# Optimization experiments

Hardware: AMD Instinct MI355X
Metric: run time of the kernel (lower is better)

Reference implementation:

```python
import jax, jax.numpy as jnp
import numpy as np

N, E, F_IN, EDGE_DIM = 50000, 800000, 128, 64
H, C = 4, 64  # heads, per-head out channels
NEG_SLOPE = 0.2  # PyG GATConv default


def setup_inputs() -> dict:
    key = jax.random.key(0)
    ks = jax.random.split(key, 16)
    p = lambda i, shape: jax.random.normal(ks[i], shape, jnp.float32) * 0.05
    return {
        "node_features": jax.random.normal(ks[0], (N, F_IN), jnp.float32),
        "edge_features": jax.random.normal(ks[1], (E, EDGE_DIM), jnp.float32),
        "edge_index": jax.random.randint(ks[2], (2, E), 0, N),
        # layer 1 (concat=True, ELU)
        "W1": p(3, (F_IN, H * C)),
        "att_src1": p(4, (H, C)), "att_dst1": p(5, (H, C)), "att_edge1": p(6, (H, C)),
        "bias1": jnp.zeros((H * C,), jnp.float32),
        "edgeW1": p(7, (EDGE_DIM, H * C)),
        # layer 2 (concat=False -> mean over heads, no activation)
        "W2": p(8, (H * C, H * C)),
        "att_src2": p(9, (H, C)), "att_dst2": p(10, (H, C)), "att_edge2": p(11, (H, C)),
        "bias2": jnp.zeros((C,), jnp.float32),
        "edgeW2": p(12, (EDGE_DIM, H * C)),
    }


def _gat_layer(x, edge_feat, src, dst, W, a_s, a_d, a_e, bias, edgeW, concat):
    n = x.shape[0]
    h = (x @ W).reshape(n, H, C)                      # [N,H,C]
    ef = (edge_feat @ edgeW).reshape(-1, H, C)        # [E,H,C] edge_linear projection
    # GATConv add_self_loops=True, fill_value='mean': self-loop attr = mean of incoming edge attrs
    ones = jnp.ones((src.shape[0],), x.dtype)
    cnt = jnp.maximum(jax.ops.segment_sum(ones, dst, num_segments=n), 1.0)
    loop_attr = jax.ops.segment_sum(ef, dst, num_segments=n) / cnt[:, None, None]
    ef_f = jnp.concatenate([ef, loop_attr], axis=0)   # [E+N,H,C]
    loops = jnp.arange(n)
    src_f = jnp.concatenate([src, loops], axis=0)
    dst_f = jnp.concatenate([dst, loops], axis=0)
    # per-edge attention logits: alpha_j + alpha_i + alpha_edge
    a_src = jnp.einsum('nhc,hc->nh', h, a_s)
    a_dst = jnp.einsum('nhc,hc->nh', h, a_d)
    logits = a_src[src_f] + a_dst[dst_f] + jnp.einsum('ehc,hc->eh', ef_f, a_e)
    logits = jax.nn.leaky_relu(logits, NEG_SLOPE)     # [E+N,H]
    # segment softmax over incoming edges of each dst node (every node has a self-loop)
    m = jax.ops.segment_max(logits, dst_f, num_segments=n)
    pexp = jnp.exp(logits - m[dst_f])
    denom = jax.ops.segment_sum(pexp, dst_f, num_segments=n)
    alpha = pexp / (denom[dst_f] + 1e-16)
    # message = x_j * alpha, scatter-add to dst
    out = jax.ops.segment_sum(h[src_f] * alpha[..., None], dst_f, num_segments=n)  # [N,H,C]
    if concat:
        return out.reshape(n, H * C) + bias
    return out.mean(axis=1) + bias


def reference(node_features, edge_features, edge_index,
              W1, att_src1, att_dst1, att_edge1, bias1, edgeW1,
              W2, att_src2, att_dst2, att_edge2, bias2, edgeW2):
    src, dst = edge_index[0], edge_index[1]
    x = _gat_layer(node_features, edge_features, src, dst,
                   W1, att_src1, att_dst1, att_edge1, bias1, edgeW1, concat=True)
    x = jax.nn.elu(x)
    return _gat_layer(x, edge_features, src, dst,
                      W2, att_src2, att_dst2, att_edge2, bias2, edgeW2, concat=False)
```

## Files before the change

kernel.cpp:

```cpp
#include <hip/hip_runtime.h>
#include <hip/hip_fp16.h>
#include <math.h>

#define NNODE 50000
#define NEDGE 800000
#define FIN 128
#define EDIM 64
#define HC 256
#define NH 4
#define CC 64
#define SCAN_TILE 512

typedef _Float16 half8v __attribute__((ext_vector_type(8)));
typedef _Float16 half4v __attribute__((ext_vector_type(4)));
typedef float floatx4 __attribute__((ext_vector_type(4)));

__global__ __launch_bounds__(256) void k_prep(int* counts, int* cursor,
                                              const float* __restrict__ W1, _Float16* wt1,
                                              const float* __restrict__ W2, _Float16* wt2,
                                              const float* __restrict__ eW1, const float* __restrict__ ae1, float* we1,
                                              const float* __restrict__ eW2, const float* __restrict__ ae2, float* we2) {
    int b = blockIdx.x, t = threadIdx.x;
    if (b < 391) {
        int i = b * 256 + t;
        if (i < NNODE) counts[i] = 0;
        else if (i < 2 * NNODE) cursor[i - NNODE] = 0;
    } else if (b < 519) {
        int idx = (b - 391) * 256 + t;
        int n = idx >> 7, k = idx & 127;
        wt1[n * FIN + k] = (_Float16)W1[(size_t)k * HC + n];
    } else if (b < 775) {
        int idx = (b - 519) * 256 + t;
        int n = idx >> 8, k = idx & 255;
        wt2[n * HC + k] = (_Float16)W2[(size_t)k * HC + n];
    } else {
        int idx = (b - 775) * 256 + t;
        const float* eW = idx < 256 ? eW1 : eW2;
        const float* ae = idx < 256 ? ae1 : ae2;
        float* we = idx < 256 ? we1 : we2;
        int q = idx & 255;
        int d = q >> 2, hh = q & 3;
        float s = 0.f;
        for (int c = 0; c < 64; c++) s += eW[d * HC + hh * 64 + c] * ae[hh * 64 + c];
        we[d * 4 + hh] = s;
    }
}

__global__ void k_count(const int* __restrict__ dst, int* counts, int E) {
    int e = blockIdx.x * 256 + threadIdx.x;
    if (e < E) atomicAdd(&counts[dst[e]], 1);
}

__global__ void k_scan1(const int* __restrict__ counts, int* offs, int* tilesums, int N) {
    __shared__ int s[SCAN_TILE];
    int t = threadIdx.x;
    int i = blockIdx.x * SCAN_TILE + t;
    int v = (i < N) ? counts[i] : 0;
    s[t] = v;
    for (int off = 1; off < SCAN_TILE; off <<= 1) {
        __syncthreads();
        int x = (t >= off) ? s[t - off] : 0;
        __syncthreads();
        s[t] += x;
    }
    __syncthreads();
    if (i < N) offs[i] = s[t] - v;
    if (t == SCAN_TILE - 1) tilesums[blockIdx.x] = s[t];
}

__global__ void k_scan2(int* tilesums, int nt) {
    __shared__ int s[128];
    int t = threadIdx.x;
    int v = (t < nt) ? tilesums[t] : 0;
    s[t] = v;
    for (int off = 1; off < 128; off <<= 1) {
        __syncthreads();
        int x = (t >= off) ? s[t - off] : 0;
        __syncthreads();
        s[t] += x;
    }
    __syncthreads();
    if (t < nt) tilesums[t] = s[t] - v;
}

__global__ void k_scan3(int* offs, const int* __restrict__ tilesums, int N, int E) {
    int t = threadIdx.x;
    int i = blockIdx.x * SCAN_TILE + t;
    if (i < N) offs[i] += tilesums[blockIdx.x];
    if (i == 0) offs[N] = E;
}

__global__ void k_fill(const int* __restrict__ src, const int* __restrict__ dst,
                       const int* __restrict__ offs, int* cursor,
                       int2* __restrict__ es, int E) {
    int e = blockIdx.x * 256 + threadIdx.x;
    if (e < E) {
        int d = dst[e];
        int pos = offs[d] + atomicAdd(&cursor[d], 1);
        es[pos] = make_int2(e, src[e]);
    }
}

__device__ inline float4 h4_to_f4(uint2 r) {
    float2 fa = __half22float2(*(__half2*)&r.x);
    float2 fb = __half22float2(*(__half2*)&r.y);
    return make_float4(fa.x, fa.y, fb.x, fb.y);
}

__device__ inline float sel_h(float4 v, int head) {
    return head == 0 ? v.x : head == 1 ? v.y : head == 2 ? v.z : v.w;
}

template <typename AT>
__global__ __launch_bounds__(256) void k_gemm_mfma(const AT* __restrict__ A,
                                                   const _Float16* __restrict__ Wt16,
                                                   _Float16* __restrict__ H16,
                                                   const float* __restrict__ att_s,
                                                   const float* __restrict__ att_d,
                                                   float* __restrict__ asrc,
                                                   float* __restrict__ adst,
                                                   int M, int K) {
    int wave = threadIdx.x >> 6, lane = threadIdx.x & 63;
    int quad = lane >> 4, l16 = lane & 15;
    int row = blockIdx.x * 64 + wave * 16 + l16;
    bool rok = row < M;
    floatx4 acc[16];
#pragma unroll
    for (int i = 0; i < 16; i++) acc[i] = (floatx4)(0.0f);
    int nk = K >> 5;
    for (int kk = 0; kk < nk; kk++) {
        half8v a = {};
        if (rok) {
            if constexpr (sizeof(AT) == 2) {
                a = *(const half8v*)(A + (size_t)row * K + kk * 32 + quad * 8);
            } else {
                const float* ap = (const float*)A + (size_t)row * K + kk * 32 + quad * 8;
                float4 v0 = *(const float4*)ap;
                float4 v1 = *(const float4*)(ap + 4);
                a[0] = (_Float16)v0.x; a[1] = (_Float16)v0.y;
                a[2] = (_Float16)v0.z; a[3] = (_Float16)v0.w;
                a[4] = (_Float16)v1.x; a[5] = (_Float16)v1.y;
                a[6] = (_Float16)v1.z; a[7] = (_Float16)v1.w;
            }
        }
#pragma unroll
        for (int nt = 0; nt < 16; nt++) {
            half8v b = *(const half8v*)(Wt16 + (size_t)(nt * 16 + l16) * K + kk * 32 + quad * 8);
            acc[nt] = __builtin_amdgcn_mfma_f32_16x16x32_f16(a, b, acc[nt], 0, 0, 0);
        }
    }
    float asl[16], adl[16];
#pragma unroll
    for (int nt = 0; nt < 16; nt++) {
        asl[nt] = att_s[nt * 16 + l16];
        adl[nt] = att_d[nt * 16 + l16];
    }
    int orow0 = blockIdx.x * 64 + wave * 16 + quad * 4;
#pragma unroll
    for (int r = 0; r < 4; r++) {
        int orow = orow0 + r;
        float4 vs4, vd4;
        float* vsp = (float*)&vs4;
        float* vdp = (float*)&vd4;
#pragma unroll
        for (int hh = 0; hh < 4; hh++) {
            float vs = 0.f, vd = 0.f;
#pragma unroll
            for (int q = 0; q < 4; q++) {
                int nt = hh * 4 + q;
                float hv = acc[nt][r];
                vs += hv * asl[nt];
                vd += hv * adl[nt];
            }
            vs += __shfl_xor(vs, 1, 64); vd += __shfl_xor(vd, 1, 64);
            vs += __shfl_xor(vs, 2, 64); vd += __shfl_xor(vd, 2, 64);
            vs += __shfl_xor(vs, 4, 64); vd += __shfl_xor(vd, 4, 64);
            vs += __shfl_xor(vs, 8, 64); vd += __shfl_xor(vd, 8, 64);
            vsp[hh] = vs; vdp[hh] = vd;
        }
        if (l16 == 0 && orow < M) {
            ((float4*)asrc)[orow] = vs4;
            ((float4*)adst)[orow] = vd4;
        }
    }
#pragma unroll
    for (int r = 0; r < 4; r++) {
        int orow = orow0 + r;
        if (orow < M) {
#pragma unroll
            for (int nt = 0; nt < 16; nt++)
                H16[(size_t)orow * HC + nt * 16 + l16] = (_Float16)acc[nt][r];
        }
    }
}

__global__ __launch_bounds__(256) void k_elog_both(const float* __restrict__ ef,
                                                   const float* __restrict__ we1,
                                                   const float* __restrict__ we2,
                                                   const int2* __restrict__ es,
                                                   float* __restrict__ elogc1,
                                                   float* __restrict__ elogc2, int E) {
    __shared__ float sw1[256], sw2[256];
    int t = threadIdx.x;
    sw1[t] = we1[t];
    sw2[t] = we2[t];
    __syncthreads();
    int p = blockIdx.x * 256 + t;
    if (p >= E) return;
    int e = es[p].x;
    const float4* row = (const float4*)(ef + (size_t)(uint)e * EDIM);
    float a10 = 0.f, a11 = 0.f, a12 = 0.f, a13 = 0.f;
    float a20 = 0.f, a21 = 0.f, a22 = 0.f, a23 = 0.f;
#pragma unroll
    for (int c4 = 0; c4 < 16; c4++) {
        float4 v = row[c4];
        const float* vp = (const float*)&v;
#pragma unroll
        for (int k = 0; k < 4; k++) {
            float vv = vp[k];
            int c = c4 * 4 + k;
            float4 w1 = *(const float4*)&sw1[c << 2];
            float4 w2 = *(const float4*)&sw2[c << 2];
            a10 += vv * w1.x; a11 += vv * w1.y; a12 += vv * w1.z; a13 += vv * w1.w;
            a20 += vv * w2.x; a21 += vv * w2.y; a22 += vv * w2.z; a23 += vv * w2.w;
        }
    }
    ((float4*)elogc1)[p] = make_float4(a10, a11, a12, a13);
    ((float4*)elogc2)[p] = make_float4(a20, a21, a22, a23);
}

template <int LAYER>
__global__ __launch_bounds__(256) void k_aggr_fused(const _Float16* __restrict__ hb,
                                                    const float* __restrict__ elogc,
                                                    const float* __restrict__ asrc,
                                                    const float* __restrict__ adst,
                                                    const int* __restrict__ offs,
                                                    const int2* __restrict__ es,
                                                    const float* __restrict__ bias,
                                                    _Float16* __restrict__ out16,
                                                    float* __restrict__ out32, int N) {
    __shared__ float sW[4][256];
    int wave = threadIdx.x >> 6, lane = threadIdx.x & 63;
    int n = blockIdx.x * 4 + wave;
    if (n >= N) return;
    int head = lane >> 4;
    const uint2* hf = (const uint2*)hb;
    const float4* elc = (const float4*)elogc;
    const float4* asp = (const float4*)asrc;
    float* sWp = sW[wave];
    int beg = offs[n], end = offs[n + 1];

    float4 adn = ((const float4*)adst)[n];
    float adnh = sel_h(adn, head);

    float denom = 0.f;
    float sx = 0.f, sy = 0.f, sz = 0.f, sw = 0.f;
    float ax = 0.f, ay = 0.f, az = 0.f, aw = 0.f;

    for (int i0 = beg; i0 < end; i0 += 64) {
        int m = end - i0; if (m > 64) m = 64;
        bool act = lane < m;
        int sj = 0;
        float4 el = make_float4(0.f, 0.f, 0.f, 0.f);
        float4 a4 = make_float4(0.f, 0.f, 0.f, 0.f);
        if (act) {
            uint idx = (uint)(i0 + lane);
            sj = es[idx].y;
            el = elc[idx];
            a4 = asp[(uint)sj];
        }
        sx += el.x; sy += el.y; sz += el.z; sw += el.w;
        float4 w4;
        float l;
        l = a4.x + adn.x + el.x; l = l > 0.f ? l : 0.2f * l; w4.x = act ? __expf(l) : 0.f;
        l = a4.y + adn.y + el.y; l = l > 0.f ? l : 0.2f * l; w4.y = act ? __expf(l) : 0.f;
        l = a4.z + adn.z + el.z; l = l > 0.f ? l : 0.2f * l; w4.z = act ? __expf(l) : 0.f;
        l = a4.w + adn.w + el.w; l = l > 0.f ? l : 0.2f * l; w4.w = act ? __expf(l) : 0.f;
        *(float4*)&sWp[lane << 2] = w4;
        __builtin_amdgcn_wave_barrier();

        int j = 0;
        for (; j + 16 <= m; j += 16) {
            uint2 r[16];
            float w[16];
#pragma unroll
            for (int k = 0; k < 16; k++) {
                int sk = __builtin_amdgcn_readlane(sj, j + k);
                w[k] = sWp[((j + k) << 2) + head];
                r[k] = hf[(size_t)((uint)sk * 64u) + lane];
            }
#pragma unroll
            for (int k = 0; k < 16; k++) {
                float4 h4 = h4_to_f4(r[k]);
                denom += w[k];
                ax += w[k] * h4.x; ay += w[k] * h4.y;
                az += w[k] * h4.z; aw += w[k] * h4.w;
            }
        }
        for (; j + 8 <= m; j += 8) {
            uint2 r[8];
            float w[8];
#pragma unroll
            for (int k = 0; k < 8; k++) {
                int sk = __builtin_amdgcn_readlane(sj, j + k);
                w[k] = sWp[((j + k) << 2) + head];
                r[k] = hf[(size_t)((uint)sk * 64u) + lane];
            }
#pragma unroll
            for (int k = 0; k < 8; k++) {
                float4 h4 = h4_to_f4(r[k]);
                denom += w[k];
                ax += w[k] * h4.x; ay += w[k] * h4.y;
                az += w[k] * h4.z; aw += w[k] * h4.w;
            }
        }
        for (; j < m; j++) {
            int sk = __builtin_amdgcn_readlane(sj, j);
            float wk = sWp[(j << 2) + head];
            uint2 rk = hf[(size_t)((uint)sk * 64u) + lane];
            float4 h4 = h4_to_f4(rk);
            denom += wk;
            ax += wk * h4.x; ay += wk * h4.y;
            az += wk * h4.z; aw += wk * h4.w;
        }
        __builtin_amdgcn_wave_barrier();
    }

#pragma unroll
    for (int msk = 32; msk >= 1; msk >>= 1) {
        sx += __shfl_xor(sx, msk, 64);
        sy += __shfl_xor(sy, msk, 64);
        sz += __shfl_xor(sz, msk, 64);
        sw += __shfl_xor(sw, msk, 64);
    }
    float selh = sel_h(make_float4(sx, sy, sz, sw), head);

    float cnt = (float)(end - beg);
    if (cnt < 1.f) cnt = 1.f;
    float asnh = sel_h(asp[(uint)n], head);
    float ls = asnh + adnh + selh / cnt;
    ls = ls > 0.f ? ls : 0.2f * ls;
    float ws = __expf(ls);
    denom += ws;
    float4 hn = h4_to_f4(hf[(size_t)n * 64 + lane]);
    ax += ws * hn.x; ay += ws * hn.y; az += ws * hn.z; aw += ws * hn.w;

    float inv = 1.0f / (denom + 1e-16f);
    ax *= inv; ay *= inv; az *= inv; aw *= inv;

    if (LAYER == 1) {
        float4 bv = ((const float4*)bias)[lane];
        half4v o;
        float v;
        v = ax + bv.x; o[0] = (_Float16)(v > 0.f ? v : __expf(v) - 1.0f);
        v = ay + bv.y; o[1] = (_Float16)(v > 0.f ? v : __expf(v) - 1.0f);
        v = az + bv.z; o[2] = (_Float16)(v > 0.f ? v : __expf(v) - 1.0f);
        v = aw + bv.w; o[3] = (_Float16)(v > 0.f ? v : __expf(v) - 1.0f);
        ((half4v*)(out16 + (size_t)n * HC))[lane] = o;
    } else {
        ax += __shfl_xor(ax, 16, 64); ax += __shfl_xor(ax, 32, 64);
        ay += __shfl_xor(ay, 16, 64); ay += __shfl_xor(ay, 32, 64);
        az += __shfl_xor(az, 16, 64); az += __shfl_xor(az, 32, 64);
        aw += __shfl_xor(aw, 16, 64); aw += __shfl_xor(aw, 32, 64);
        if (lane < 16) {
            float4 bv = ((const float4*)bias)[lane];
            float4 o;
            o.x = 0.25f * ax + bv.x;
            o.y = 0.25f * ay + bv.y;
            o.z = 0.25f * az + bv.z;
            o.w = 0.25f * aw + bv.w;
            ((float4*)(out32 + (size_t)n * CC))[lane] = o;
        }
    }
}

extern "C" void kernel_launch(void* const* d_in, const int* in_sizes, int n_in,
                              void* d_out, int out_size, void* d_ws, size_t ws_size,
                              hipStream_t stream) {
    const float* x   = (const float*)d_in[0];
    const float* ef  = (const float*)d_in[1];
    const int*   ei  = (const int*)d_in[2];
    const float* W1  = (const float*)d_in[3];
    const float* as1 = (const float*)d_in[4];
    const float* ad1 = (const float*)d_in[5];
    const float* ae1 = (const float*)d_in[6];
    const float* b1  = (const float*)d_in[7];
    const float* eW1 = (const float*)d_in[8];
    const float* W2  = (const float*)d_in[9];
    const float* as2 = (const float*)d_in[10];
    const float* ad2 = (const float*)d_in[11];
    const float* ae2 = (const float*)d_in[12];
    const float* b2  = (const float*)d_in[13];
    const float* eW2 = (const float*)d_in[14];
    float* out = (float*)d_out;
    const int* srcp = ei;
    const int* dstp = ei + NEDGE;

    char* w = (char*)d_ws;
    auto alloc = [&](size_t bytes) -> char* {
        char* r = w;
        w += (bytes + 255) / 256 * 256;
        return r;
    };
    _Float16* hb16  = (_Float16*)alloc((size_t)NNODE * HC * 2);
    _Float16* x216  = (_Float16*)alloc((size_t)NNODE * HC * 2);
    _Float16* wt1   = (_Float16*)alloc((size_t)HC * FIN * 2);
    _Float16* wt2   = (_Float16*)alloc((size_t)HC * HC * 2);
    float* elogc1 = (float*)alloc((size_t)NEDGE * 4 * 4);
    float* elogc2 = (float*)alloc((size_t)NEDGE * 4 * 4);
    float* asrc   = (float*)alloc((size_t)NNODE * 4 * 4);
    float* adst   = (float*)alloc((size_t)NNODE * 4 * 4);
    float* webuf1 = (float*)alloc(64 * 4 * 4);
    float* webuf2 = (float*)alloc(64 * 4 * 4);
    int* counts  = (int*)alloc((size_t)NNODE * 4);
    int* offs    = (int*)alloc((size_t)(NNODE + 1) * 4);
    int* tiles   = (int*)alloc(1024 * 4);
    int* cursor  = (int*)alloc((size_t)NNODE * 4);
    int2* es     = (int2*)alloc((size_t)NEDGE * 8);

    k_prep<<<777, 256, 0, stream>>>(counts, cursor, W1, wt1, W2, wt2,
                                    eW1, ae1, webuf1, eW2, ae2, webuf2);

    k_count<<<(NEDGE + 255) / 256, 256, 0, stream>>>(dstp, counts, NEDGE);
    int nt = (NNODE + SCAN_TILE - 1) / SCAN_TILE;
    k_scan1<<<nt, SCAN_TILE, 0, stream>>>(counts, offs, tiles, NNODE);
    k_scan2<<<1, 128, 0, stream>>>(tiles, nt);
    k_scan3<<<nt, SCAN_TILE, 0, stream>>>(offs, tiles, NNODE, NEDGE);
    k_fill<<<(NEDGE + 255) / 256, 256, 0, stream>>>(srcp, dstp, offs, cursor, es, NEDGE);

    k_elog_both<<<(NEDGE + 255) / 256, 256, 0, stream>>>(ef, webuf1, webuf2, es, elogc1, elogc2, NEDGE);

    k_gemm_mfma<float><<<(NNODE + 63) / 64, 256, 0, stream>>>(x, wt1, hb16, as1, ad1, asrc, adst, NNODE, FIN);
    k_aggr_fused<1><<<(NNODE + 3) / 4, 256, 0, stream>>>(hb16, elogc1, asrc, adst, offs, es, b1, x216, nullptr, NNODE);

    k_gemm_mfma<_Float16><<<(NNODE + 63) / 64, 256, 0, stream>>>(x216, wt2, hb16, as2, ad2, asrc, adst, NNODE, HC);
    k_aggr_fused<2><<<(NNODE + 3) / 4, 256, 0, stream>>>(hb16, elogc2, asrc, adst, offs, es, b2, nullptr, out, NNODE);
}
```

Baseline: 702.9 us.

## Record atomic rank in count pass and fuse CSR fill with edge-logit computation

```diff
diff --git a/kernel.cpp b/kernel.cpp
--- a/kernel.cpp
+++ b/kernel.cpp
@@ -15,26 +15,25 @@
 typedef _Float16 half4v __attribute__((ext_vector_type(4)));
 typedef float floatx4 __attribute__((ext_vector_type(4)));
 
-__global__ __launch_bounds__(256) void k_prep(int* counts, int* cursor,
+__global__ __launch_bounds__(256) void k_prep(int* counts,
                                               const float* __restrict__ W1, _Float16* wt1,
                                               const float* __restrict__ W2, _Float16* wt2,
                                               const float* __restrict__ eW1, const float* __restrict__ ae1, float* we1,
                                               const float* __restrict__ eW2, const float* __restrict__ ae2, float* we2) {
     int b = blockIdx.x, t = threadIdx.x;
-    if (b < 391) {
+    if (b < 196) {
         int i = b * 256 + t;
         if (i < NNODE) counts[i] = 0;
-        else if (i < 2 * NNODE) cursor[i - NNODE] = 0;
-    } else if (b < 519) {
-        int idx = (b - 391) * 256 + t;
+    } else if (b < 324) {
+        int idx = (b - 196) * 256 + t;
         int n = idx >> 7, k = idx & 127;
         wt1[n * FIN + k] = (_Float16)W1[(size_t)k * HC + n];
-    } else if (b < 775) {
-        int idx = (b - 519) * 256 + t;
+    } else if (b < 580) {
+        int idx = (b - 324) * 256 + t;
         int n = idx >> 8, k = idx & 255;
         wt2[n * HC + k] = (_Float16)W2[(size_t)k * HC + n];
     } else {
-        int idx = (b - 775) * 256 + t;
+        int idx = (b - 580) * 256 + t;
         const float* eW = idx < 256 ? eW1 : eW2;
         const float* ae = idx < 256 ? ae1 : ae2;
         float* we = idx < 256 ? we1 : we2;
@@ -46,9 +45,9 @@
     }
 }
 
-__global__ void k_count(const int* __restrict__ dst, int* counts, int E) {
+__global__ void k_count(const int* __restrict__ dst, int* counts, int* __restrict__ rank, int E) {
     int e = blockIdx.x * 256 + threadIdx.x;
-    if (e < E) atomicAdd(&counts[dst[e]], 1);
+    if (e < E) rank[e] = atomicAdd(&counts[dst[e]], 1);
 }
 
 __global__ void k_scan1(const int* __restrict__ counts, int* offs, int* tilesums, int N) {
@@ -68,37 +67,17 @@
     if (t == SCAN_TILE - 1) tilesums[blockIdx.x] = s[t];
 }
 
-__global__ void k_scan2(int* tilesums, int nt) {
-    __shared__ int s[128];
+__global__ void k_scan3(int* offs, const int* __restrict__ tilesums, int nt, int N, int E) {
+    __shared__ int sT[128];
     int t = threadIdx.x;
-    int v = (t < nt) ? tilesums[t] : 0;
-    s[t] = v;
-    for (int off = 1; off < 128; off <<= 1) {
-        __syncthreads();
-        int x = (t >= off) ? s[t - off] : 0;
-        __syncthreads();
-        s[t] += x;
-    }
+    if (t < 128) sT[t] = (t < nt) ? tilesums[t] : 0;
     __syncthreads();
-    if (t < nt) tilesums[t] = s[t] - v;
-}
-
-__global__ void k_scan3(int* offs, const int* __restrict__ tilesums, int N, int E) {
-    int t = threadIdx.x;
-    int i = blockIdx.x * SCAN_TILE + t;
-    if (i < N) offs[i] += tilesums[blockIdx.x];
-    if (i == 0) offs[N] = E;
-}
-
-__global__ void k_fill(const int* __restrict__ src, const int* __restrict__ dst,
-                       const int* __restrict__ offs, int* cursor,
-                       int2* __restrict__ es, int E) {
-    int e = blockIdx.x * 256 + threadIdx.x;
-    if (e < E) {
-        int d = dst[e];
-        int pos = offs[d] + atomicAdd(&cursor[d], 1);
-        es[pos] = make_int2(e, src[e]);
-    }
+    int b = blockIdx.x;
+    int pre = 0;
+    for (int i = 0; i < b; i++) pre += sT[i];
+    int i = b * SCAN_TILE + t;
+    if (i < N) offs[i] += pre;
+    if (b == 0 && t == 0) offs[N] = E;
 }
 
 __device__ inline float4 h4_to_f4(uint2 r) {
@@ -109,6 +88,46 @@
 
 __device__ inline float sel_h(float4 v, int head) {
     return head == 0 ? v.x : head == 1 ? v.y : head == 2 ? v.z : v.w;
+}
+
+__global__ __launch_bounds__(256) void k_edge(const int* __restrict__ src,
+                                              const int* __restrict__ dst,
+                                              const int* __restrict__ rank,
+                                              const int* __restrict__ offs,
+                                              const float* __restrict__ ef,
+                                              const float* __restrict__ we1,
+                                              const float* __restrict__ we2,
+                                              int* __restrict__ srcs,
+                                              float* __restrict__ elogc1,
+                                              float* __restrict__ elogc2, int E) {
+    __shared__ float sw1[256], sw2[256];
+    int t = threadIdx.x;
+    sw1[t] = we1[t];
+    sw2[t] = we2[t];
+    __syncthreads();
+    int e = blockIdx.x * 256 + t;
+    if (e >= E) return;
+    int pos = offs[dst[e]] + rank[e];
+    srcs[pos] = src[e];
+    const float4* row = (const float4*)(ef + (size_t)e * EDIM);
+    float a10 = 0.f, a11 = 0.f, a12 = 0.f, a13 = 0.f;
+    float a20 = 0.f, a21 = 0.f, a22 = 0.f, a23 = 0.f;
+#pragma unroll
+    for (int c4 = 0; c4 < 16; c4++) {
+        float4 v = row[c4];
+        const float* vp = (const float*)&v;
+#pragma unroll
+        for (int k = 0; k < 4; k++) {
+            float vv = vp[k];
+            int c = c4 * 4 + k;
+            float4 w1 = *(const float4*)&sw1[c << 2];
+            float4 w2 = *(const float4*)&sw2[c << 2];
+            a10 += vv * w1.x; a11 += vv * w1.y; a12 += vv * w1.z; a13 += vv * w1.w;
+            a20 += vv * w2.x; a21 += vv * w2.y; a22 += vv * w2.z; a23 += vv * w2.w;
+        }
+    }
+    ((float4*)elogc1)[pos] = make_float4(a10, a11, a12, a13);
+    ((float4*)elogc2)[pos] = make_float4(a20, a21, a22, a23);
 }
 
 template <typename AT>
@@ -194,48 +213,13 @@
     }
 }
 
-__global__ __launch_bounds__(256) void k_elog_both(const float* __restrict__ ef,
-                                                   const float* __restrict__ we1,
-                                                   const float* __restrict__ we2,
-                                                   const int2* __restrict__ es,
-                                                   float* __restrict__ elogc1,
-                                                   float* __restrict__ elogc2, int E) {
-    __shared__ float sw1[256], sw2[256];
-    int t = threadIdx.x;
-    sw1[t] = we1[t];
-    sw2[t] = we2[t];
-    __syncthreads();
-    int p = blockIdx.x * 256 + t;
-    if (p >= E) return;
-    int e = es[p].x;
-    const float4* row = (const float4*)(ef + (size_t)(uint)e * EDIM);
-    float a10 = 0.f, a11 = 0.f, a12 = 0.f, a13 = 0.f;
-    float a20 = 0.f, a21 = 0.f, a22 = 0.f, a23 = 0.f;
-#pragma unroll
-    for (int c4 = 0; c4 < 16; c4++) {
-        float4 v = row[c4];
-        const float* vp = (const float*)&v;
-#pragma unroll
-        for (int k = 0; k < 4; k++) {
-            float vv = vp[k];
-            int c = c4 * 4 + k;
-            float4 w1 = *(const float4*)&sw1[c << 2];
-            float4 w2 = *(const float4*)&sw2[c << 2];
-            a10 += vv * w1.x; a11 += vv * w1.y; a12 += vv * w1.z; a13 += vv * w1.w;
-            a20 += vv * w2.x; a21 += vv * w2.y; a22 += vv * w2.z; a23 += vv * w2.w;
-        }
-    }
-    ((float4*)elogc1)[p] = make_float4(a10, a11, a12, a13);
-    ((float4*)elogc2)[p] = make_float4(a20, a21, a22, a23);
-}
-
 template <int LAYER>
 __global__ __launch_bounds__(256) void k_aggr_fused(const _Float16* __restrict__ hb,
                                                     const float* __restrict__ elogc,
                                                     const float* __restrict__ asrc,
                                                     const float* __restrict__ adst,
                                                     const int* __restrict__ offs,
-                                                    const int2* __restrict__ es,
+                                                    const int* __restrict__ srcs,
                                                     const float* __restrict__ bias,
                                                     _Float16* __restrict__ out16,
                                                     float* __restrict__ out32, int N) {
@@ -265,7 +249,7 @@
         float4 a4 = make_float4(0.f, 0.f, 0.f, 0.f);
         if (act) {
             uint idx = (uint)(i0 + lane);
-            sj = es[idx].y;
+            sj = srcs[idx];
             el = elc[idx];
             a4 = asp[(uint)sj];
         }
@@ -415,24 +399,23 @@
     int* counts  = (int*)alloc((size_t)NNODE * 4);
     int* offs    = (int*)alloc((size_t)(NNODE + 1) * 4);
     int* tiles   = (int*)alloc(1024 * 4);
-    int* cursor  = (int*)alloc((size_t)NNODE * 4);
-    int2* es     = (int2*)alloc((size_t)NEDGE * 8);
-
-    k_prep<<<777, 256, 0, stream>>>(counts, cursor, W1, wt1, W2, wt2,
+    int* rank    = (int*)alloc((size_t)NEDGE * 4);
+    int* srcs    = (int*)alloc((size_t)NEDGE * 4);
+
+    k_prep<<<582, 256, 0, stream>>>(counts, W1, wt1, W2, wt2,
                                     eW1, ae1, webuf1, eW2, ae2, webuf2);
 
-    k_count<<<(NEDGE + 255) / 256, 256, 0, stream>>>(dstp, counts, NEDGE);
+    k_count<<<(NEDGE + 255) / 256, 256, 0, stream>>>(dstp, counts, rank, NEDGE);
     int nt = (NNODE + SCAN_TILE - 1) / SCAN_TILE;
     k_scan1<<<nt, SCAN_TILE, 0, stream>>>(counts, offs, tiles, NNODE);
-    k_scan2<<<1, 128, 0, stream>>>(tiles, nt);
-    k_scan3<<<nt, SCAN_TILE, 0, stream>>>(offs, tiles, NNODE, NEDGE);
-    k_fill<<<(NEDGE + 255) / 256, 256, 0, stream>>>(srcp, dstp, offs, cursor, es, NEDGE);
-
-    k_elog_both<<<(NEDGE + 255) / 256, 256, 0, stream>>>(ef, webuf1, webuf2, es, elogc1, elogc2, NEDGE);
+    k_scan3<<<nt, SCAN_TILE, 0, stream>>>(offs, tiles, nt, NNODE, NEDGE);
+
+    k_edge<<<(NEDGE + 255) / 256, 256, 0, stream>>>(srcp, dstp, rank, offs, ef,
+                                                    webuf1, webuf2, srcs, elogc1, elogc2, NEDGE);
 
     k_gemm_mfma<float><<<(NNODE + 63) / 64, 256, 0, stream>>>(x, wt1, hb16, as1, ad1, asrc, adst, NNODE, FIN);
-    k_aggr_fused<1><<<(NNODE + 3) / 4, 256, 0, stream>>>(hb16, elogc1, asrc, adst, offs, es, b1, x216, nullptr, NNODE);
+    k_aggr_fused<1><<<(NNODE + 3) / 4, 256, 0, stream>>>(hb16, elogc1, asrc, adst, offs, srcs, b1, x216, nullptr, NNODE);
 
     k_gemm_mfma<_Float16><<<(NNODE + 63) / 64, 256, 0, stream>>>(x216, wt2, hb16, as2, ad2, asrc, adst, NNODE, HC);
-    k_aggr_fused<2><<<(NNODE + 3) / 4, 256, 0, stream>>>(hb16, elogc2, asrc, adst, offs, es, b2, nullptr, out, NNODE);
-}
+    k_aggr_fused<2><<<(NNODE + 3) / 4, 256, 0, stream>>>(hb16, elogc2, asrc, adst, offs, srcs, b2, nullptr, out, NNODE);
+}
```

New measurement: 692.7 us. Within noise of the previous version (-1.4%).
